# Performance work log

Hardware: AMD Instinct MI355X
Metric: run time of the kernel (lower is better)

## Reference

```python
import jax, jax.numpy as jnp
import numpy as np

N_NODES = 200000
N_EDGES = 600000
FP = 128


def _gru_cell(x, h, wih, whh, bih, bhh):
    # torch.nn.GRUCell: gates ordered (r, z, n)
    gi = x @ wih.T + bih
    gh = h @ whh.T + bhh
    ir, iz, inn = jnp.split(gi, 3, axis=-1)
    hr, hz, hn = jnp.split(gh, 3, axis=-1)
    r = jax.nn.sigmoid(ir + hr)
    z = jax.nn.sigmoid(iz + hz)
    n = jnp.tanh(inn + r * hn)
    return (1.0 - z) * n + z * h


def _layer(x, dst, step, aw, ab, tw, tb, wih, whh, bih, bhh):
    n_nodes = x.shape[0]
    x_i = x[dst]  # [E, F] gather of target-node features
    if step == 0:
        h_s = jnp.broadcast_to(jnp.sum(x_i, axis=-1, keepdims=True), x_i.shape)
    else:
        h_s = x_i
    esv = jax.nn.leaky_relu(jnp.concatenate([h_s, x_i], axis=-1) @ aw.T + ab)  # [E,1]
    asv = jax.nn.softmax(esv, axis=-1)  # size-1 softmax -> ones (faithful)
    cs = jax.nn.elu(asv * (h_s @ tw.T + tb))  # dropout is identity at eval
    m = _gru_cell(cs, h_s, wih, whh, bih, bhh)  # per-edge GRU update [E,F]
    return jax.ops.segment_sum(m, dst, num_segments=n_nodes)  # scatter-add aggregate


def setup_inputs() -> dict:
    key = jax.random.key(0)
    ks = jax.random.split(key, 20)
    s = 1.0 / np.sqrt(FP)
    inp = {
        "x": jax.random.normal(ks[0], (N_NODES, FP), dtype=jnp.float32),
        "edge_index": jax.random.randint(ks[1], (2, N_EDGES), 0, N_NODES, dtype=jnp.int64),
    }
    i = 2
    for l in range(2):
        inp[f"align_w{l}"] = jax.random.uniform(ks[i], (1, 2 * FP), jnp.float32, -s, s); i += 1
        inp[f"align_b{l}"] = jax.random.uniform(ks[i], (1,), jnp.float32, -s, s); i += 1
        inp[f"attend_w{l}"] = jax.random.uniform(ks[i], (FP, FP), jnp.float32, -s, s); i += 1
        inp[f"attend_b{l}"] = jax.random.uniform(ks[i], (FP,), jnp.float32, -s, s); i += 1
        inp[f"wih{l}"] = jax.random.uniform(ks[i], (3 * FP, FP), jnp.float32, -s, s); i += 1
        inp[f"whh{l}"] = jax.random.uniform(ks[i], (3 * FP, FP), jnp.float32, -s, s); i += 1
        inp[f"bih{l}"] = jax.random.uniform(ks[i], (3 * FP,), jnp.float32, -s, s); i += 1
        inp[f"bhh{l}"] = jax.random.uniform(ks[i], (3 * FP,), jnp.float32, -s, s); i += 1
    return inp


def reference(x, edge_index,
              align_w0, align_b0, attend_w0, attend_b0, wih0, whh0, bih0, bhh0,
              align_w1, align_b1, attend_w1, attend_b1, wih1, whh1, bih1, bhh1):
    dst = edge_index[1]
    x = _layer(x, dst, 0, align_w0, align_b0, attend_w0, attend_b0, wih0, whh0, bih0, bhh0)
    x = _layer(x, dst, 1, align_w1, align_b1, attend_w1, attend_b1, wih1, whh1, bih1, bhh1)
    return x
```

## Files before the change

### kernel.cpp

```cpp
#include <hip/hip_runtime.h>
#include <cmath>

#define NN 200000
#define NE 600000

typedef __bf16 bf16x8 __attribute__((ext_vector_type(8)));
typedef float f32x4 __attribute__((ext_vector_type(4)));

#define LOG2E 1.44269504088896340736f
__device__ __forceinline__ float fexp2(float x) { return __builtin_amdgcn_exp2f(x); }
__device__ __forceinline__ float frcp(float x) { return __builtin_amdgcn_rcpf(x); }
__device__ __forceinline__ float sigm(float v) { return frcp(1.0f + fexp2(-LOG2E * v)); }
__device__ __forceinline__ float ftanh(float v) {
  float t = fexp2(-2.0f * LOG2E * fabsf(v));
  float r = (1.0f - t) * frcp(1.0f + t);
  return __builtin_copysignf(r, v);
}
__device__ __forceinline__ float eluf(float v) { return v > 0.0f ? v : fexp2(LOG2E * v) - 1.0f; }

__device__ __forceinline__ unsigned short bfr(float f) {
  unsigned u = __float_as_uint(f);
  u += 0x7FFFu + ((u >> 16) & 1u);
  return (unsigned short)(u >> 16);
}
__device__ __forceinline__ void bsplit(float v, unsigned short& hi, unsigned short& lo) {
  unsigned short h = bfr(v);
  float hf = __uint_as_float(((unsigned)h) << 16);
  hi = h;
  lo = bfr(v - hf);
}


__global__ __launch_bounds__(256) void hist_kernel(const int* __restrict__ dst,
                                                   int* __restrict__ deg) {
  int e = blockIdx.x * 256 + threadIdx.x;
  if (e < NE) atomicAdd(&deg[dst[e]], 1);
}

__global__ __launch_bounds__(512) void prep_kernel(const float* __restrict__ attw0,
                                                   const float* __restrict__ whh0,
                                                   float* __restrict__ rwt0,
                                                   float* __restrict__ rwh0) {
  int t = threadIdx.x;
  if (t < 128) {
    float s = 0.f;
    for (int k = 0; k < 128; k++) s += attw0[t * 128 + k];
    rwt0[t] = s;
  } else {
    int j = t - 128;
    float s = 0.f;
    for (int k = 0; k < 128; k++) s += whh0[j * 128 + k];
    rwh0[j] = s;
  }
}

__global__ __launch_bounds__(256) void pack_kernel(
    const float* __restrict__ wih0, const float* __restrict__ tw1,
    const float* __restrict__ wih1, const float* __restrict__ whh1,
    unsigned short* __restrict__ w0ph, unsigned short* __restrict__ w0pl,
    unsigned short* __restrict__ w1ph, unsigned short* __restrict__ w1pl,
    unsigned short* __restrict__ w2ph, unsigned short* __restrict__ w2pl) {
  int g = blockIdx.x * 256 + threadIdx.x;
  unsigned short *PH, *PL;
  const float* row;
  int l;
  if (g < 6144) { l = g; PH = w0ph; PL = w0pl; }
  else if (g < 8192) { l = g - 6144; PH = w1ph; PL = w1pl; }
  else if (g < 20480) { l = g - 8192; PH = w2ph; PL = w2pl; }
  else return;
  int lane = l & 63, ks = (l >> 6) & 3, nt = l >> 8;
  int n = nt * 16 + (lane & 15);
  int k0 = ks * 32 + (lane >> 4) * 8;
  if (g < 6144) row = wih0 + n * 128;
  else if (g < 8192) row = tw1 + n * 128;
  else row = (n < 384) ? wih1 + n * 128 : whh1 + (n - 384) * 128;
  unsigned uh[4], ul[4];
  for (int p = 0; p < 4; p++) {
    unsigned short ah, al, bh, bl;
    bsplit(row[k0 + 2 * p], ah, al);
    bsplit(row[k0 + 2 * p + 1], bh, bl);
    uh[p] = (unsigned)ah | ((unsigned)bh << 16);
    ul[p] = (unsigned)al | ((unsigned)bl << 16);
  }
  *(uint4*)&PH[l * 8] = make_uint4(uh[0], uh[1], uh[2], uh[3]);
  *(uint4*)&PL[l * 8] = make_uint4(ul[0], ul[1], ul[2], ul[3]);
}

#define MFMA3(accv, ah, al, bh, bl)                                          \
  accv = __builtin_amdgcn_mfma_f32_16x16x32_bf16(ah, bh, accv, 0, 0, 0);     \
  accv = __builtin_amdgcn_mfma_f32_16x16x32_bf16(ah, bl, accv, 0, 0, 0);     \
  accv = __builtin_amdgcn_mfma_f32_16x16x32_bf16(al, bh, accv, 0, 0, 0);

__global__ __launch_bounds__(512, 4) void layer0_kernel(
    const float* __restrict__ x, const float* __restrict__ tb0,
    const unsigned short* __restrict__ w0ph, const unsigned short* __restrict__ w0pl,
    const float* __restrict__ bih0, const float* __restrict__ bhh0,
    const float* __restrict__ rwt0, const float* __restrict__ rwh0,
    const int* __restrict__ deg, float* __restrict__ x1) {
  __shared__ float s_lds[64];
  __shared__ float deg_lds[64];
  __shared__ unsigned short csh[64 * 136];
  __shared__ unsigned short csl[64 * 136];

  const int tid = threadIdx.x;
  const int lane = tid & 63;
  const int wv = tid >> 6;
  const int n0 = blockIdx.x * 64;

  if (tid < 64) deg_lds[tid] = (float)deg[n0 + tid];

  {
    int m = tid >> 3, c = (tid & 7) * 16;
    const float4* xr = (const float4*)(x + (size_t)(n0 + m) * 128 + c);
    float a = 0.f;
#pragma unroll
    for (int q = 0; q < 4; q++) { float4 v = xr[q]; a += v.x + v.y + v.z + v.w; }
#pragma unroll
    for (int o = 1; o < 8; o <<= 1) a += __shfl_xor(a, o, 64);
    if ((tid & 7) == 0) s_lds[m] = a;
  }
  __syncthreads();

  {
    int m = tid >> 3, c0 = (tid & 7) * 16;
    float s = s_lds[m];
#pragma unroll
    for (int q = 0; q < 4; q++) {
      int k = c0 + q * 4;
      unsigned short h0, l0, h1, l1, h2, l2, h3, l3;
      bsplit(eluf(fmaf(s, rwt0[k], tb0[k])), h0, l0);
      bsplit(eluf(fmaf(s, rwt0[k + 1], tb0[k + 1])), h1, l1);
      bsplit(eluf(fmaf(s, rwt0[k + 2], tb0[k + 2])), h2, l2);
      bsplit(eluf(fmaf(s, rwt0[k + 3], tb0[k + 3])), h3, l3);
      *(uint2*)&csh[m * 136 + k] =
          make_uint2((unsigned)h0 | ((unsigned)h1 << 16), (unsigned)h2 | ((unsigned)h3 << 16));
      *(uint2*)&csl[m * 136 + k] =
          make_uint2((unsigned)l0 | ((unsigned)l1 << 16), (unsigned)l2 | ((unsigned)l3 << 16));
    }
  }
  __syncthreads();

  const int mrow = lane & 15;
  const int kq = (lane >> 4) * 8;
  const int quad = lane >> 4;
  f32x4 acc[4][3] = {};
#pragma unroll
  for (int ks = 0; ks < 4; ks++) {
    bf16x8 ah[4], al[4];
#pragma unroll
    for (int mt = 0; mt < 4; mt++) {
      ah[mt] = *(const bf16x8*)&csh[(mt * 16 + mrow) * 136 + ks * 32 + kq];
      al[mt] = *(const bf16x8*)&csl[(mt * 16 + mrow) * 136 + ks * 32 + kq];
    }
#pragma unroll
    for (int g = 0; g < 3; g++) {
      int nt = g * 8 + wv;
      size_t base = (size_t)((nt * 4 + ks) * 64 + lane) * 8;
      bf16x8 bh = *(const bf16x8*)&w0ph[base];
      bf16x8 bl = *(const bf16x8*)&w0pl[base];
#pragma unroll
      for (int mt = 0; mt < 4; mt++) { MFMA3(acc[mt][g], ah[mt], al[mt], bh, bl); }
    }
  }

  const int j = wv * 16 + mrow;
  float bir = bih0[j], biz = bih0[j + 128], bin_ = bih0[j + 256];
  float bhr = bhh0[j], bhz = bhh0[j + 128], bhn = bhh0[j + 256];
  float rwr = rwh0[j], rwz = rwh0[j + 128], rwn = rwh0[j + 256];
#pragma unroll
  for (int mt = 0; mt < 4; mt++) {
#pragma unroll
    for (int reg = 0; reg < 4; reg++) {
      int m = mt * 16 + quad * 4 + reg;
      float s = s_lds[m];
      float dd = deg_lds[m];
      float gir = acc[mt][0][reg] + bir;
      float giz = acc[mt][1][reg] + biz;
      float gin = acc[mt][2][reg] + bin_;
      float ghr = fmaf(s, rwr, bhr);
      float ghz = fmaf(s, rwz, bhz);
      float ghn = fmaf(s, rwn, bhn);
      float r = sigm(gir + ghr);
      float z = sigm(giz + ghz);
      float nn2 = ftanh(fmaf(r, ghn, gin));
      x1[(size_t)(n0 + m) * 128 + j] = dd * ((1.f - z) * nn2 + z * s);
    }
  }
}

__global__ __launch_bounds__(512, 2) void layer1_kernel(
    const float* __restrict__ x1, const float* __restrict__ tb1,
    const unsigned short* __restrict__ w1ph, const unsigned short* __restrict__ w1pl,
    const unsigned short* __restrict__ w2ph, const unsigned short* __restrict__ w2pl,
    const float* __restrict__ bih1, const float* __restrict__ bhh1,
    const int* __restrict__ deg, float* __restrict__ out) {
  extern __shared__ unsigned short smem[];
  unsigned short* hh = smem;
  unsigned short* hl = smem + 8704;
  unsigned short* ch = smem + 17408;
  unsigned short* cl = smem + 26112;
  __shared__ float deg_lds[64];

  const int tid = threadIdx.x;
  const int lane = tid & 63;
  const int wv = tid >> 6;
  const int n0 = blockIdx.x * 64;
  const int mrow = lane & 15;
  const int kq = (lane >> 4) * 8;
  const int quad = lane >> 4;

  if (tid < 64) deg_lds[tid] = (float)deg[n0 + tid];

  {
    int m = tid >> 3, c0 = (tid & 7) * 16;
    const float4* xr = (const float4*)(x1 + (size_t)(n0 + m) * 128 + c0);
#pragma unroll
    for (int q = 0; q < 4; q++) {
      float4 v = xr[q];
      unsigned short h0, l0, h1, l1, h2, l2, h3, l3;
      bsplit(v.x, h0, l0); bsplit(v.y, h1, l1);
      bsplit(v.z, h2, l2); bsplit(v.w, h3, l3);
      *(uint2*)&hh[m * 136 + c0 + q * 4] =
          make_uint2((unsigned)h0 | ((unsigned)h1 << 16), (unsigned)h2 | ((unsigned)h3 << 16));
      *(uint2*)&hl[m * 136 + c0 + q * 4] =
          make_uint2((unsigned)l0 | ((unsigned)l1 << 16), (unsigned)l2 | ((unsigned)l3 << 16));
    }
  }
  __syncthreads();

  f32x4 acc1[4] = {};
  f32x4 acc2[4][6] = {};
#pragma unroll
  for (int ks = 0; ks < 4; ks++) {
    bf16x8 xh[4], xl[4];
#pragma unroll
    for (int mt = 0; mt < 4; mt++) {
      xh[mt] = *(const bf16x8*)&hh[(mt * 16 + mrow) * 136 + ks * 32 + kq];
      xl[mt] = *(const bf16x8*)&hl[(mt * 16 + mrow) * 136 + ks * 32 + kq];
    }
    {
      size_t base = (size_t)((wv * 4 + ks) * 64 + lane) * 8;
      bf16x8 bh = *(const bf16x8*)&w1ph[base];
      bf16x8 bl = *(const bf16x8*)&w1pl[base];
#pragma unroll
      for (int mt = 0; mt < 4; mt++) { MFMA3(acc1[mt], xh[mt], xl[mt], bh, bl); }
    }
#pragma unroll
    for (int g = 0; g < 3; g++) {
      int nt = 24 + g * 8 + wv;
      size_t base = (size_t)((nt * 4 + ks) * 64 + lane) * 8;
      bf16x8 bh = *(const bf16x8*)&w2ph[base];
      bf16x8 bl = *(const bf16x8*)&w2pl[base];
#pragma unroll
      for (int mt = 0; mt < 4; mt++) { MFMA3(acc2[mt][3 + g], xh[mt], xl[mt], bh, bl); }
    }
  }

  {
    float tbj = tb1[wv * 16 + mrow];
#pragma unroll
    for (int mt = 0; mt < 4; mt++) {
#pragma unroll
      for (int reg = 0; reg < 4; reg++) {
        int m = mt * 16 + quad * 4 + reg;
        unsigned short vh, vl;
        bsplit(eluf(acc1[mt][reg] + tbj), vh, vl);
        unsigned pv = (unsigned)vh | ((unsigned)vl << 16);
        unsigned pu = __shfl_xor(pv, 1, 64);
        if ((lane & 1) == 0) {
          int jc = wv * 16 + mrow;
          unsigned hpack = (pv & 0xFFFFu) | (pu << 16);
          unsigned lpack = (pv >> 16) | (pu & 0xFFFF0000u);
          *(unsigned*)&ch[m * 136 + jc] = hpack;
          *(unsigned*)&cl[m * 136 + jc] = lpack;
        }
      }
    }
  }
  __syncthreads();

#pragma unroll
  for (int ks = 0; ks < 4; ks++) {
    bf16x8 ah[4], al[4];
#pragma unroll
    for (int mt = 0; mt < 4; mt++) {
      ah[mt] = *(const bf16x8*)&ch[(mt * 16 + mrow) * 136 + ks * 32 + kq];
      al[mt] = *(const bf16x8*)&cl[(mt * 16 + mrow) * 136 + ks * 32 + kq];
    }
#pragma unroll
    for (int g = 0; g < 3; g++) {
      int nt = g * 8 + wv;
      size_t base = (size_t)((nt * 4 + ks) * 64 + lane) * 8;
      bf16x8 bh = *(const bf16x8*)&w2ph[base];
      bf16x8 bl = *(const bf16x8*)&w2pl[base];
#pragma unroll
      for (int mt = 0; mt < 4; mt++) { MFMA3(acc2[mt][g], ah[mt], al[mt], bh, bl); }
    }
  }

  const int j = wv * 16 + mrow;
  float bir = bih1[j], biz = bih1[j + 128], bin_ = bih1[j + 256];
  float bhr = bhh1[j], bhz = bhh1[j + 128], bhn = bhh1[j + 256];
#pragma unroll
  for (int mt = 0; mt < 4; mt++) {
#pragma unroll
    for (int reg = 0; reg < 4; reg++) {
      int m = mt * 16 + quad * 4 + reg;
      float dd = deg_lds[m];
      float gir = acc2[mt][0][reg] + bir;
      float giz = acc2[mt][1][reg] + biz;
      float gin = acc2[mt][2][reg] + bin_;
      float ghr = acc2[mt][3][reg] + bhr;
      float ghz = acc2[mt][4][reg] + bhz;
      float ghn = acc2[mt][5][reg] + bhn;
      float r = sigm(gir + ghr);
      float z = sigm(giz + ghz);
      float nn2 = ftanh(fmaf(r, ghn, gin));
      float hfull = (float)(*(const __bf16*)&hh[m * 136 + j]) +
                    (float)(*(const __bf16*)&hl[m * 136 + j]);
      out[(size_t)(n0 + m) * 128 + j] = dd * ((1.f - z) * nn2 + z * hfull);
    }
  }
}

extern "C" void kernel_launch(void* const* d_in, const int* in_sizes, int n_in,
                              void* d_out, int out_size, void* d_ws, size_t ws_size,
                              hipStream_t stream) {
  const float* x     = (const float*)d_in[0];
  const int*   edge  = (const int*)d_in[1];
  const float* attw0 = (const float*)d_in[4];
  const float* attb0 = (const float*)d_in[5];
  const float* wih0  = (const float*)d_in[6];
  const float* whh0  = (const float*)d_in[7];
  const float* bih0  = (const float*)d_in[8];
  const float* bhh0  = (const float*)d_in[9];
  const float* attw1 = (const float*)d_in[12];
  const float* attb1 = (const float*)d_in[13];
  const float* wih1  = (const float*)d_in[14];
  const float* whh1  = (const float*)d_in[15];
  const float* bih1  = (const float*)d_in[16];
  const float* bhh1  = (const float*)d_in[17];

  float* ws   = (float*)d_ws;
  float* x1   = ws;
  int*   deg  = (int*)(ws + 25600000);
  float* rwt0 = ws + 25800000;
  float* rwh0 = ws + 25800128;
  unsigned short* wp = (unsigned short*)(ws + 25800512);
  unsigned short* w0ph = wp;
  unsigned short* w0pl = wp + 49152;
  unsigned short* w1ph = wp + 98304;
  unsigned short* w1pl = wp + 114688;
  unsigned short* w2ph = wp + 131072;
  unsigned short* w2pl = wp + 229376;

  const int* dst = edge + NE;

  static bool attr_done = false;
  if (!attr_done) {
    hipFuncSetAttribute(reinterpret_cast<const void*>(layer1_kernel),
                        hipFuncAttributeMaxDynamicSharedMemorySize, 69632);
    attr_done = true;
  }

  hipMemsetAsync(deg, 0, NN * sizeof(int), stream);
  hist_kernel<<<(NE + 255) / 256, 256, 0, stream>>>(dst, deg);
  prep_kernel<<<1, 512, 0, stream>>>(attw0, whh0, rwt0, rwh0);
  pack_kernel<<<80, 256, 0, stream>>>(wih0, attw1, wih1, whh1,
                                      w0ph, w0pl, w1ph, w1pl, w2ph, w2pl);
  layer0_kernel<<<NN / 64, 512, 0, stream>>>(x, attb0, w0ph, w0pl, bih0, bhh0,
                                             rwt0, rwh0, deg, x1);
  layer1_kernel<<<NN / 64, 512, 69632, stream>>>(x1, attb1, w1ph, w1pl, w2ph, w2pl,
                                                 bih1, bhh1, deg, (float*)d_out);
}
```

Measured before the change: 450.1 us.

## Retile layer1 to 128-node blocks with 2D wave grid; parallelize row-sum prep

layer1 now processes 128 nodes per 1024-thread block, with the 16 waves arranged as a 4x4 grid over rows and output columns instead of each wave covering all rows of one column slice. The two GEMMs are interleaved per k-step, and the r/z gates sum the input and hidden accumulators directly, using 4 accumulator groups instead of 6. This is meant to cut weight re-fetches per node and lower register pressure, at the cost of doubling LDS to 136 KB per block, which limits occupancy to one block per CU, and adding tail bounds checks. The one-block prep kernel is also replaced by a wave-per-row shuffle reduction spread over 128 blocks.

```diff
diff --git a/kernel.cpp b/kernel.cpp
--- a/kernel.cpp
+++ b/kernel.cpp
@@ -37,20 +37,21 @@
   if (e < NE) atomicAdd(&deg[dst[e]], 1);
 }
 
-__global__ __launch_bounds__(512) void prep_kernel(const float* __restrict__ attw0,
+__global__ __launch_bounds__(256) void prep_kernel(const float* __restrict__ attw0,
                                                    const float* __restrict__ whh0,
                                                    float* __restrict__ rwt0,
                                                    float* __restrict__ rwh0) {
-  int t = threadIdx.x;
-  if (t < 128) {
-    float s = 0.f;
-    for (int k = 0; k < 128; k++) s += attw0[t * 128 + k];
-    rwt0[t] = s;
-  } else {
-    int j = t - 128;
-    float s = 0.f;
-    for (int k = 0; k < 128; k++) s += whh0[j * 128 + k];
-    rwh0[j] = s;
+  int gw = blockIdx.x * 4 + (threadIdx.x >> 6);
+  int lane = threadIdx.x & 63;
+  const float* row = (gw < 128) ? (attw0 + (size_t)gw * 128)
+                                : (whh0 + (size_t)(gw - 128) * 128);
+  float2 v = ((const float2*)row)[lane];
+  float a = v.x + v.y;
+#pragma unroll
+  for (int o = 1; o < 64; o <<= 1) a += __shfl_xor(a, o, 64);
+  if (lane == 0) {
+    if (gw < 128) rwt0[gw] = a;
+    else rwh0[gw - 128] = a;
   }
 }
 
@@ -188,7 +189,7 @@
   }
 }
 
-__global__ __launch_bounds__(512, 2) void layer1_kernel(
+__global__ __launch_bounds__(1024) void layer1_kernel(
     const float* __restrict__ x1, const float* __restrict__ tb1,
     const unsigned short* __restrict__ w1ph, const unsigned short* __restrict__ w1pl,
     const unsigned short* __restrict__ w2ph, const unsigned short* __restrict__ w2pl,
@@ -196,24 +197,31 @@
     const int* __restrict__ deg, float* __restrict__ out) {
   extern __shared__ unsigned short smem[];
   unsigned short* hh = smem;
-  unsigned short* hl = smem + 8704;
-  unsigned short* ch = smem + 17408;
-  unsigned short* cl = smem + 26112;
-  __shared__ float deg_lds[64];
+  unsigned short* hl = smem + 17408;
+  unsigned short* ch = smem + 34816;
+  unsigned short* cl = smem + 52224;
+  __shared__ float deg_lds[128];
 
   const int tid = threadIdx.x;
   const int lane = tid & 63;
   const int wv = tid >> 6;
-  const int n0 = blockIdx.x * 64;
+  const int mg = wv >> 2;
+  const int ng = wv & 3;
+  const int n0 = blockIdx.x * 128;
   const int mrow = lane & 15;
   const int kq = (lane >> 4) * 8;
   const int quad = lane >> 4;
 
-  if (tid < 64) deg_lds[tid] = (float)deg[n0 + tid];
+  if (tid < 128) {
+    int node = n0 + tid;
+    deg_lds[tid] = (node < NN) ? (float)deg[node] : 0.f;
+  }
 
   {
     int m = tid >> 3, c0 = (tid & 7) * 16;
-    const float4* xr = (const float4*)(x1 + (size_t)(n0 + m) * 128 + c0);
+    int node = n0 + m;
+    if (node >= NN) node = NN - 1;
+    const float4* xr = (const float4*)(x1 + (size_t)node * 128 + c0);
 #pragma unroll
     for (int q = 0; q < 4; q++) {
       float4 v = xr[q];
@@ -228,97 +236,132 @@
   }
   __syncthreads();
 
-  f32x4 acc1[4] = {};
-  f32x4 acc2[4][6] = {};
+  const int r0 = mg * 32;
+  const int c0w = ng * 32;
+
+  f32x4 acc1[2][2] = {};
 #pragma unroll
   for (int ks = 0; ks < 4; ks++) {
-    bf16x8 xh[4], xl[4];
-#pragma unroll
-    for (int mt = 0; mt < 4; mt++) {
-      xh[mt] = *(const bf16x8*)&hh[(mt * 16 + mrow) * 136 + ks * 32 + kq];
-      xl[mt] = *(const bf16x8*)&hl[(mt * 16 + mrow) * 136 + ks * 32 + kq];
-    }
-    {
-      size_t base = (size_t)((wv * 4 + ks) * 64 + lane) * 8;
+    bf16x8 xh[2], xl[2];
+#pragma unroll
+    for (int mt = 0; mt < 2; mt++) {
+      xh[mt] = *(const bf16x8*)&hh[(r0 + mt * 16 + mrow) * 136 + ks * 32 + kq];
+      xl[mt] = *(const bf16x8*)&hl[(r0 + mt * 16 + mrow) * 136 + ks * 32 + kq];
+    }
+#pragma unroll
+    for (int sub = 0; sub < 2; sub++) {
+      int nt = ng * 2 + sub;
+      size_t base = (size_t)((nt * 4 + ks) * 64 + lane) * 8;
       bf16x8 bh = *(const bf16x8*)&w1ph[base];
       bf16x8 bl = *(const bf16x8*)&w1pl[base];
 #pragma unroll
-      for (int mt = 0; mt < 4; mt++) { MFMA3(acc1[mt], xh[mt], xl[mt], bh, bl); }
-    }
-#pragma unroll
-    for (int g = 0; g < 3; g++) {
-      int nt = 24 + g * 8 + wv;
-      size_t base = (size_t)((nt * 4 + ks) * 64 + lane) * 8;
-      bf16x8 bh = *(const bf16x8*)&w2ph[base];
-      bf16x8 bl = *(const bf16x8*)&w2pl[base];
-#pragma unroll
-      for (int mt = 0; mt < 4; mt++) { MFMA3(acc2[mt][3 + g], xh[mt], xl[mt], bh, bl); }
+      for (int mt = 0; mt < 2; mt++) { MFMA3(acc1[mt][sub], xh[mt], xl[mt], bh, bl); }
     }
   }
 
   {
-    float tbj = tb1[wv * 16 + mrow];
-#pragma unroll
-    for (int mt = 0; mt < 4; mt++) {
-#pragma unroll
-      for (int reg = 0; reg < 4; reg++) {
-        int m = mt * 16 + quad * 4 + reg;
-        unsigned short vh, vl;
-        bsplit(eluf(acc1[mt][reg] + tbj), vh, vl);
-        unsigned pv = (unsigned)vh | ((unsigned)vl << 16);
-        unsigned pu = __shfl_xor(pv, 1, 64);
-        if ((lane & 1) == 0) {
-          int jc = wv * 16 + mrow;
-          unsigned hpack = (pv & 0xFFFFu) | (pu << 16);
-          unsigned lpack = (pv >> 16) | (pu & 0xFFFF0000u);
-          *(unsigned*)&ch[m * 136 + jc] = hpack;
-          *(unsigned*)&cl[m * 136 + jc] = lpack;
+    float tbj[2];
+#pragma unroll
+    for (int sub = 0; sub < 2; sub++) tbj[sub] = tb1[c0w + sub * 16 + mrow];
+#pragma unroll
+    for (int mt = 0; mt < 2; mt++) {
+#pragma unroll
+      for (int sub = 0; sub < 2; sub++) {
+#pragma unroll
+        for (int reg = 0; reg < 4; reg++) {
+          int m = r0 + mt * 16 + quad * 4 + reg;
+          unsigned short vh, vl;
+          bsplit(eluf(acc1[mt][sub][reg] + tbj[sub]), vh, vl);
+          unsigned pv = (unsigned)vh | ((unsigned)vl << 16);
+          unsigned pu = __shfl_xor(pv, 1, 64);
+          if ((lane & 1) == 0) {
+            int jc = c0w + sub * 16 + mrow;
+            unsigned hpack = (pv & 0xFFFFu) | (pu << 16);
+            unsigned lpack = (pv >> 16) | (pu & 0xFFFF0000u);
+            *(unsigned*)&ch[m * 136 + jc] = hpack;
+            *(unsigned*)&cl[m * 136 + jc] = lpack;
+          }
         }
       }
     }
   }
   __syncthreads();
 
+  f32x4 acc2[2][2][4] = {};
 #pragma unroll
   for (int ks = 0; ks < 4; ks++) {
-    bf16x8 ah[4], al[4];
-#pragma unroll
-    for (int mt = 0; mt < 4; mt++) {
-      ah[mt] = *(const bf16x8*)&ch[(mt * 16 + mrow) * 136 + ks * 32 + kq];
-      al[mt] = *(const bf16x8*)&cl[(mt * 16 + mrow) * 136 + ks * 32 + kq];
-    }
-#pragma unroll
-    for (int g = 0; g < 3; g++) {
-      int nt = g * 8 + wv;
-      size_t base = (size_t)((nt * 4 + ks) * 64 + lane) * 8;
-      bf16x8 bh = *(const bf16x8*)&w2ph[base];
-      bf16x8 bl = *(const bf16x8*)&w2pl[base];
-#pragma unroll
-      for (int mt = 0; mt < 4; mt++) { MFMA3(acc2[mt][g], ah[mt], al[mt], bh, bl); }
-    }
-  }
-
-  const int j = wv * 16 + mrow;
-  float bir = bih1[j], biz = bih1[j + 128], bin_ = bih1[j + 256];
-  float bhr = bhh1[j], bhz = bhh1[j + 128], bhn = bhh1[j + 256];
-#pragma unroll
-  for (int mt = 0; mt < 4; mt++) {
+    {
+      bf16x8 xh[2], xl[2];
+#pragma unroll
+      for (int mt = 0; mt < 2; mt++) {
+        xh[mt] = *(const bf16x8*)&hh[(r0 + mt * 16 + mrow) * 136 + ks * 32 + kq];
+        xl[mt] = *(const bf16x8*)&hl[(r0 + mt * 16 + mrow) * 136 + ks * 32 + kq];
+      }
+#pragma unroll
+      for (int sub = 0; sub < 2; sub++) {
+#pragma unroll
+        for (int g = 0; g < 3; g++) {
+          int nt = 24 + g * 8 + ng * 2 + sub;
+          size_t base = (size_t)((nt * 4 + ks) * 64 + lane) * 8;
+          bf16x8 bh = *(const bf16x8*)&w2ph[base];
+          bf16x8 bl = *(const bf16x8*)&w2pl[base];
+          int grp = (g == 2) ? 3 : g;
+#pragma unroll
+          for (int mt = 0; mt < 2; mt++) { MFMA3(acc2[mt][sub][grp], xh[mt], xl[mt], bh, bl); }
+        }
+      }
+    }
+    {
+      bf16x8 ah[2], al[2];
+#pragma unroll
+      for (int mt = 0; mt < 2; mt++) {
+        ah[mt] = *(const bf16x8*)&ch[(r0 + mt * 16 + mrow) * 136 + ks * 32 + kq];
+        al[mt] = *(const bf16x8*)&cl[(r0 + mt * 16 + mrow) * 136 + ks * 32 + kq];
+      }
+#pragma unroll
+      for (int sub = 0; sub < 2; sub++) {
+#pragma unroll
+        for (int g = 0; g < 3; g++) {
+          int nt = g * 8 + ng * 2 + sub;
+          size_t base = (size_t)((nt * 4 + ks) * 64 + lane) * 8;
+          bf16x8 bh = *(const bf16x8*)&w2ph[base];
+          bf16x8 bl = *(const bf16x8*)&w2pl[base];
+#pragma unroll
+          for (int mt = 0; mt < 2; mt++) { MFMA3(acc2[mt][sub][g], ah[mt], al[mt], bh, bl); }
+        }
+      }
+    }
+  }
+
+  float bir[2], biz[2], bin_[2], bhr[2], bhz[2], bhn[2];
+  int jcol[2];
+#pragma unroll
+  for (int sub = 0; sub < 2; sub++) {
+    int j = c0w + sub * 16 + mrow;
+    jcol[sub] = j;
+    bir[sub] = bih1[j]; biz[sub] = bih1[j + 128]; bin_[sub] = bih1[j + 256];
+    bhr[sub] = bhh1[j]; bhz[sub] = bhh1[j + 128]; bhn[sub] = bhh1[j + 256];
+  }
+#pragma unroll
+  for (int mt = 0; mt < 2; mt++) {
 #pragma unroll
     for (int reg = 0; reg < 4; reg++) {
-      int m = mt * 16 + quad * 4 + reg;
+      int m = r0 + mt * 16 + quad * 4 + reg;
+      int node = n0 + m;
       float dd = deg_lds[m];
-      float gir = acc2[mt][0][reg] + bir;
-      float giz = acc2[mt][1][reg] + biz;
-      float gin = acc2[mt][2][reg] + bin_;
-      float ghr = acc2[mt][3][reg] + bhr;
-      float ghz = acc2[mt][4][reg] + bhz;
-      float ghn = acc2[mt][5][reg] + bhn;
-      float r = sigm(gir + ghr);
-      float z = sigm(giz + ghz);
-      float nn2 = ftanh(fmaf(r, ghn, gin));
-      float hfull = (float)(*(const __bf16*)&hh[m * 136 + j]) +
-                    (float)(*(const __bf16*)&hl[m * 136 + j]);
-      out[(size_t)(n0 + m) * 128 + j] = dd * ((1.f - z) * nn2 + z * hfull);
+#pragma unroll
+      for (int sub = 0; sub < 2; sub++) {
+        int j = jcol[sub];
+        float r = sigm(acc2[mt][sub][0][reg] + bir[sub] + bhr[sub]);
+        float z = sigm(acc2[mt][sub][1][reg] + biz[sub] + bhz[sub]);
+        float ghn = acc2[mt][sub][3][reg] + bhn[sub];
+        float gin = acc2[mt][sub][2][reg] + bin_[sub];
+        float nn2 = ftanh(fmaf(r, ghn, gin));
+        float hfull = (float)(*(const __bf16*)&hh[m * 136 + j]) +
+                      (float)(*(const __bf16*)&hl[m * 136 + j]);
+        if (node < NN)
+          out[(size_t)node * 128 + j] = dd * ((1.f - z) * nn2 + z * hfull);
+      }
     }
   }
 }
@@ -359,17 +402,17 @@
   static bool attr_done = false;
   if (!attr_done) {
     hipFuncSetAttribute(reinterpret_cast<const void*>(layer1_kernel),
-                        hipFuncAttributeMaxDynamicSharedMemorySize, 69632);
+                        hipFuncAttributeMaxDynamicSharedMemorySize, 139264);
     attr_done = true;
   }
 
   hipMemsetAsync(deg, 0, NN * sizeof(int), stream);
   hist_kernel<<<(NE + 255) / 256, 256, 0, stream>>>(dst, deg);
-  prep_kernel<<<1, 512, 0, stream>>>(attw0, whh0, rwt0, rwh0);
+  prep_kernel<<<128, 256, 0, stream>>>(attw0, whh0, rwt0, rwh0);
   pack_kernel<<<80, 256, 0, stream>>>(wih0, attw1, wih1, whh1,
                                       w0ph, w0pl, w1ph, w1pl, w2ph, w2pl);
   layer0_kernel<<<NN / 64, 512, 0, stream>>>(x, attb0, w0ph, w0pl, bih0, bhh0,
                                              rwt0, rwh0, deg, x1);
-  layer1_kernel<<<NN / 64, 512, 69632, stream>>>(x1, attb1, w1ph, w1pl, w2ph, w2pl,
-                                                 bih1, bhh1, deg, (float*)d_out);
-}
+  layer1_kernel<<<(NN + 127) / 128, 1024, 139264, stream>>>(
+      x1, attb1, w1ph, w1pl, w2ph, w2pl, bih1, bhh1, deg, (float*)d_out);
+}
```

Measured after the change: 489.3 us. 8.7% more time.

## Switch to 32x32x16 MFMA with fragment-packed bf16 hi/lo intermediate layout

Applied to the files above, without the earlier changes.

Replaces the 16x16x32 MFMA tiling with 32x32x16 MFMAs, with each wave computing a 32-row by 32-column tile per gate. Layer 0 now writes its output as split bf16 hi/lo halves, pre-laid out in MFMA A-fragment order. Layer 1 can then load its operands straight from global memory without the LDS staging and bsplit conversion, which cuts LDS use and allows higher occupancy. The prep kernel is also parallelised across many blocks using wave reductions. The cost is extra index arithmetic and a fixed fragment layout in the workspace.

```diff
diff --git a/kernel.cpp b/kernel.cpp
--- a/kernel.cpp
+++ b/kernel.cpp
@@ -5,7 +5,7 @@
 #define NE 600000
 
 typedef __bf16 bf16x8 __attribute__((ext_vector_type(8)));
-typedef float f32x4 __attribute__((ext_vector_type(4)));
+typedef float f32x16 __attribute__((ext_vector_type(16)));
 
 #define LOG2E 1.44269504088896340736f
 __device__ __forceinline__ float fexp2(float x) { return __builtin_amdgcn_exp2f(x); }
@@ -37,20 +37,21 @@
   if (e < NE) atomicAdd(&deg[dst[e]], 1);
 }
 
-__global__ __launch_bounds__(512) void prep_kernel(const float* __restrict__ attw0,
+__global__ __launch_bounds__(256) void prep_kernel(const float* __restrict__ attw0,
                                                    const float* __restrict__ whh0,
                                                    float* __restrict__ rwt0,
                                                    float* __restrict__ rwh0) {
-  int t = threadIdx.x;
-  if (t < 128) {
-    float s = 0.f;
-    for (int k = 0; k < 128; k++) s += attw0[t * 128 + k];
-    rwt0[t] = s;
-  } else {
-    int j = t - 128;
-    float s = 0.f;
-    for (int k = 0; k < 128; k++) s += whh0[j * 128 + k];
-    rwh0[j] = s;
+  int gw = blockIdx.x * 4 + (threadIdx.x >> 6);
+  int lane = threadIdx.x & 63;
+  const float* row = (gw < 128) ? (attw0 + (size_t)gw * 128)
+                                : (whh0 + (size_t)(gw - 128) * 128);
+  float2 v = ((const float2*)row)[lane];
+  float a = v.x + v.y;
+#pragma unroll
+  for (int o = 1; o < 64; o <<= 1) a += __shfl_xor(a, o, 64);
+  if (lane == 0) {
+    if (gw < 128) rwt0[gw] = a;
+    else rwh0[gw - 128] = a;
   }
 }
 
@@ -61,20 +62,21 @@
     unsigned short* __restrict__ w1ph, unsigned short* __restrict__ w1pl,
     unsigned short* __restrict__ w2ph, unsigned short* __restrict__ w2pl) {
   int g = blockIdx.x * 256 + threadIdx.x;
+  if (g >= 20480) return;
   unsigned short *PH, *PL;
   const float* row;
   int l;
   if (g < 6144) { l = g; PH = w0ph; PL = w0pl; }
   else if (g < 8192) { l = g - 6144; PH = w1ph; PL = w1pl; }
-  else if (g < 20480) { l = g - 8192; PH = w2ph; PL = w2pl; }
-  else return;
-  int lane = l & 63, ks = (l >> 6) & 3, nt = l >> 8;
-  int n = nt * 16 + (lane & 15);
-  int k0 = ks * 32 + (lane >> 4) * 8;
+  else { l = g - 8192; PH = w2ph; PL = w2pl; }
+  int lane = l & 63, ks = (l >> 6) & 7, nt = l >> 9;
+  int n = nt * 32 + (lane & 31);
+  int k0 = ks * 16 + (lane >> 5) * 8;
   if (g < 6144) row = wih0 + n * 128;
   else if (g < 8192) row = tw1 + n * 128;
   else row = (n < 384) ? wih1 + n * 128 : whh1 + (n - 384) * 128;
   unsigned uh[4], ul[4];
+#pragma unroll
   for (int p = 0; p < 4; p++) {
     unsigned short ah, al, bh, bl;
     bsplit(row[k0 + 2 * p], ah, al);
@@ -87,24 +89,27 @@
 }
 
 #define MFMA3(accv, ah, al, bh, bl)                                          \
-  accv = __builtin_amdgcn_mfma_f32_16x16x32_bf16(ah, bh, accv, 0, 0, 0);     \
-  accv = __builtin_amdgcn_mfma_f32_16x16x32_bf16(ah, bl, accv, 0, 0, 0);     \
-  accv = __builtin_amdgcn_mfma_f32_16x16x32_bf16(al, bh, accv, 0, 0, 0);
+  accv = __builtin_amdgcn_mfma_f32_32x32x16_bf16(ah, bh, accv, 0, 0, 0);     \
+  accv = __builtin_amdgcn_mfma_f32_32x32x16_bf16(ah, bl, accv, 0, 0, 0);     \
+  accv = __builtin_amdgcn_mfma_f32_32x32x16_bf16(al, bh, accv, 0, 0, 0);
 
 __global__ __launch_bounds__(512, 4) void layer0_kernel(
     const float* __restrict__ x, const float* __restrict__ tb0,
     const unsigned short* __restrict__ w0ph, const unsigned short* __restrict__ w0pl,
     const float* __restrict__ bih0, const float* __restrict__ bhh0,
     const float* __restrict__ rwt0, const float* __restrict__ rwh0,
-    const int* __restrict__ deg, float* __restrict__ x1) {
+    const int* __restrict__ deg,
+    unsigned short* __restrict__ x1h, unsigned short* __restrict__ x1l) {
   __shared__ float s_lds[64];
   __shared__ float deg_lds[64];
-  __shared__ unsigned short csh[64 * 136];
-  __shared__ unsigned short csl[64 * 136];
+  __shared__ unsigned short csh[8192];
+  __shared__ unsigned short csl[8192];
 
   const int tid = threadIdx.x;
   const int lane = tid & 63;
   const int wv = tid >> 6;
+  const int mg = wv & 1;
+  const int cb = wv >> 1;
   const int n0 = blockIdx.x * 64;
 
   if (tid < 64) deg_lds[tid] = (float)deg[n0 + tid];
@@ -122,204 +127,167 @@
   __syncthreads();
 
   {
-    int m = tid >> 3, c0 = (tid & 7) * 16;
+    int m = lane, c = wv;
     float s = s_lds[m];
-#pragma unroll
-    for (int q = 0; q < 4; q++) {
-      int k = c0 + q * 4;
-      unsigned short h0, l0, h1, l1, h2, l2, h3, l3;
-      bsplit(eluf(fmaf(s, rwt0[k], tb0[k])), h0, l0);
-      bsplit(eluf(fmaf(s, rwt0[k + 1], tb0[k + 1])), h1, l1);
-      bsplit(eluf(fmaf(s, rwt0[k + 2], tb0[k + 2])), h2, l2);
-      bsplit(eluf(fmaf(s, rwt0[k + 3], tb0[k + 3])), h3, l3);
-      *(uint2*)&csh[m * 136 + k] =
-          make_uint2((unsigned)h0 | ((unsigned)h1 << 16), (unsigned)h2 | ((unsigned)h3 << 16));
-      *(uint2*)&csl[m * 136 + k] =
-          make_uint2((unsigned)l0 | ((unsigned)l1 << 16), (unsigned)l2 | ((unsigned)l3 << 16));
+    int kb = c * 16;
+    int fb = (((m >> 5) * 8 + c) * 64 + (m & 31)) * 8;
+#pragma unroll
+    for (int u = 0; u < 2; u++) {
+      unsigned uh[4], ul[4];
+#pragma unroll
+      for (int p = 0; p < 4; p++) {
+        int k = kb + u * 8 + p * 2;
+        unsigned short h0, l0, h1, l1;
+        bsplit(eluf(fmaf(s, rwt0[k], tb0[k])), h0, l0);
+        bsplit(eluf(fmaf(s, rwt0[k + 1], tb0[k + 1])), h1, l1);
+        uh[p] = (unsigned)h0 | ((unsigned)h1 << 16);
+        ul[p] = (unsigned)l0 | ((unsigned)l1 << 16);
+      }
+      *(uint4*)&csh[fb + u * 256] = make_uint4(uh[0], uh[1], uh[2], uh[3]);
+      *(uint4*)&csl[fb + u * 256] = make_uint4(ul[0], ul[1], ul[2], ul[3]);
     }
   }
   __syncthreads();
 
-  const int mrow = lane & 15;
-  const int kq = (lane >> 4) * 8;
-  const int quad = lane >> 4;
-  f32x4 acc[4][3] = {};
-#pragma unroll
-  for (int ks = 0; ks < 4; ks++) {
-    bf16x8 ah[4], al[4];
-#pragma unroll
-    for (int mt = 0; mt < 4; mt++) {
-      ah[mt] = *(const bf16x8*)&csh[(mt * 16 + mrow) * 136 + ks * 32 + kq];
-      al[mt] = *(const bf16x8*)&csl[(mt * 16 + mrow) * 136 + ks * 32 + kq];
-    }
+  f32x16 acc[3] = {};
+#pragma unroll
+  for (int ks = 0; ks < 8; ks++) {
+    bf16x8 ah = *(const bf16x8*)&csh[((mg * 8 + ks) * 64 + lane) * 8];
+    bf16x8 al = *(const bf16x8*)&csl[((mg * 8 + ks) * 64 + lane) * 8];
 #pragma unroll
     for (int g = 0; g < 3; g++) {
-      int nt = g * 8 + wv;
-      size_t base = (size_t)((nt * 4 + ks) * 64 + lane) * 8;
+      int nt = g * 4 + cb;
+      size_t base = (size_t)((nt * 8 + ks) * 64 + lane) * 8;
       bf16x8 bh = *(const bf16x8*)&w0ph[base];
       bf16x8 bl = *(const bf16x8*)&w0pl[base];
-#pragma unroll
-      for (int mt = 0; mt < 4; mt++) { MFMA3(acc[mt][g], ah[mt], al[mt], bh, bl); }
-    }
-  }
-
-  const int j = wv * 16 + mrow;
-  float bir = bih0[j], biz = bih0[j + 128], bin_ = bih0[j + 256];
-  float bhr = bhh0[j], bhz = bhh0[j + 128], bhn = bhh0[j + 256];
-  float rwr = rwh0[j], rwz = rwh0[j + 128], rwn = rwh0[j + 256];
-#pragma unroll
-  for (int mt = 0; mt < 4; mt++) {
-#pragma unroll
-    for (int reg = 0; reg < 4; reg++) {
-      int m = mt * 16 + quad * 4 + reg;
-      float s = s_lds[m];
-      float dd = deg_lds[m];
-      float gir = acc[mt][0][reg] + bir;
-      float giz = acc[mt][1][reg] + biz;
-      float gin = acc[mt][2][reg] + bin_;
-      float ghr = fmaf(s, rwr, bhr);
-      float ghz = fmaf(s, rwz, bhz);
-      float ghn = fmaf(s, rwn, bhn);
-      float r = sigm(gir + ghr);
-      float z = sigm(giz + ghz);
-      float nn2 = ftanh(fmaf(r, ghn, gin));
-      x1[(size_t)(n0 + m) * 128 + j] = dd * ((1.f - z) * nn2 + z * s);
-    }
-  }
-}
-
-__global__ __launch_bounds__(512, 2) void layer1_kernel(
-    const float* __restrict__ x1, const float* __restrict__ tb1,
+      MFMA3(acc[g], ah, al, bh, bl);
+    }
+  }
+
+  const int jc = cb * 32 + (lane & 31);
+  float bir = bih0[jc], biz = bih0[jc + 128], bin_ = bih0[jc + 256];
+  float bhr = bhh0[jc], bhz = bhh0[jc + 128], bhn = bhh0[jc + 256];
+  float rwr = rwh0[jc], rwz = rwh0[jc + 128], rwn = rwh0[jc + 256];
+  const size_t tbase = (size_t)blockIdx.x * 8192;
+  const int fj = ((mg * 8 + (cb * 2 + ((lane >> 4) & 1))) * 64 + ((lane >> 3) & 1) * 32) * 8 +
+                 (lane & 7);
+#pragma unroll
+  for (int reg = 0; reg < 16; reg++) {
+    int crow = (reg & 3) + 8 * (reg >> 2) + 4 * (lane >> 5);
+    int m = mg * 32 + crow;
+    float s = s_lds[m];
+    float dd = deg_lds[m];
+    float r = sigm(acc[0][reg] + bir + fmaf(s, rwr, bhr));
+    float z = sigm(acc[1][reg] + biz + fmaf(s, rwz, bhz));
+    float nn2 = ftanh(fmaf(r, fmaf(s, rwn, bhn), acc[2][reg] + bin_));
+    float v = dd * ((1.f - z) * nn2 + z * s);
+    unsigned short vh, vl;
+    bsplit(v, vh, vl);
+    unsigned pv = (unsigned)vh | ((unsigned)vl << 16);
+    unsigned pu = __shfl_xor(pv, 1, 64);
+    if ((lane & 1) == 0) {
+      size_t f = tbase + fj + crow * 8;
+      *(unsigned*)&x1h[f] = (pv & 0xFFFFu) | (pu << 16);
+      *(unsigned*)&x1l[f] = (pv >> 16) | (pu & 0xFFFF0000u);
+    }
+  }
+}
+
+__global__ __launch_bounds__(512, 4) void layer1_kernel(
+    const unsigned short* __restrict__ x1h, const unsigned short* __restrict__ x1l,
+    const float* __restrict__ tb1,
     const unsigned short* __restrict__ w1ph, const unsigned short* __restrict__ w1pl,
     const unsigned short* __restrict__ w2ph, const unsigned short* __restrict__ w2pl,
     const float* __restrict__ bih1, const float* __restrict__ bhh1,
     const int* __restrict__ deg, float* __restrict__ out) {
-  extern __shared__ unsigned short smem[];
-  unsigned short* hh = smem;
-  unsigned short* hl = smem + 8704;
-  unsigned short* ch = smem + 17408;
-  unsigned short* cl = smem + 26112;
+  __shared__ unsigned short cfh[8192];
+  __shared__ unsigned short cfl[8192];
   __shared__ float deg_lds[64];
 
   const int tid = threadIdx.x;
   const int lane = tid & 63;
   const int wv = tid >> 6;
+  const int mg = wv & 1;
+  const int cb = wv >> 1;
   const int n0 = blockIdx.x * 64;
-  const int mrow = lane & 15;
-  const int kq = (lane >> 4) * 8;
-  const int quad = lane >> 4;
+  const size_t tbase = (size_t)blockIdx.x * 8192;
 
   if (tid < 64) deg_lds[tid] = (float)deg[n0 + tid];
 
-  {
-    int m = tid >> 3, c0 = (tid & 7) * 16;
-    const float4* xr = (const float4*)(x1 + (size_t)(n0 + m) * 128 + c0);
-#pragma unroll
-    for (int q = 0; q < 4; q++) {
-      float4 v = xr[q];
-      unsigned short h0, l0, h1, l1, h2, l2, h3, l3;
-      bsplit(v.x, h0, l0); bsplit(v.y, h1, l1);
-      bsplit(v.z, h2, l2); bsplit(v.w, h3, l3);
-      *(uint2*)&hh[m * 136 + c0 + q * 4] =
-          make_uint2((unsigned)h0 | ((unsigned)h1 << 16), (unsigned)h2 | ((unsigned)h3 << 16));
-      *(uint2*)&hl[m * 136 + c0 + q * 4] =
-          make_uint2((unsigned)l0 | ((unsigned)l1 << 16), (unsigned)l2 | ((unsigned)l3 << 16));
-    }
-  }
-  __syncthreads();
-
-  f32x4 acc1[4] = {};
-  f32x4 acc2[4][6] = {};
-#pragma unroll
-  for (int ks = 0; ks < 4; ks++) {
-    bf16x8 xh[4], xl[4];
-#pragma unroll
-    for (int mt = 0; mt < 4; mt++) {
-      xh[mt] = *(const bf16x8*)&hh[(mt * 16 + mrow) * 136 + ks * 32 + kq];
-      xl[mt] = *(const bf16x8*)&hl[(mt * 16 + mrow) * 136 + ks * 32 + kq];
-    }
+  f32x16 aA[4] = {};
+#pragma unroll
+  for (int ks = 0; ks < 8; ks++) {
+    bf16x8 ah = *(const bf16x8*)&x1h[tbase + ((mg * 8 + ks) * 64 + lane) * 8];
+    bf16x8 al = *(const bf16x8*)&x1l[tbase + ((mg * 8 + ks) * 64 + lane) * 8];
     {
-      size_t base = (size_t)((wv * 4 + ks) * 64 + lane) * 8;
+      size_t base = (size_t)((cb * 8 + ks) * 64 + lane) * 8;
       bf16x8 bh = *(const bf16x8*)&w1ph[base];
       bf16x8 bl = *(const bf16x8*)&w1pl[base];
-#pragma unroll
-      for (int mt = 0; mt < 4; mt++) { MFMA3(acc1[mt], xh[mt], xl[mt], bh, bl); }
+      MFMA3(aA[3], ah, al, bh, bl);
     }
 #pragma unroll
     for (int g = 0; g < 3; g++) {
-      int nt = 24 + g * 8 + wv;
-      size_t base = (size_t)((nt * 4 + ks) * 64 + lane) * 8;
+      int nt = 12 + g * 4 + cb;
+      size_t base = (size_t)((nt * 8 + ks) * 64 + lane) * 8;
       bf16x8 bh = *(const bf16x8*)&w2ph[base];
       bf16x8 bl = *(const bf16x8*)&w2pl[base];
-#pragma unroll
-      for (int mt = 0; mt < 4; mt++) { MFMA3(acc2[mt][3 + g], xh[mt], xl[mt], bh, bl); }
+      MFMA3(aA[g], ah, al, bh, bl);
     }
   }
 
   {
-    float tbj = tb1[wv * 16 + mrow];
-#pragma unroll
-    for (int mt = 0; mt < 4; mt++) {
-#pragma unroll
-      for (int reg = 0; reg < 4; reg++) {
-        int m = mt * 16 + quad * 4 + reg;
-        unsigned short vh, vl;
-        bsplit(eluf(acc1[mt][reg] + tbj), vh, vl);
-        unsigned pv = (unsigned)vh | ((unsigned)vl << 16);
-        unsigned pu = __shfl_xor(pv, 1, 64);
-        if ((lane & 1) == 0) {
-          int jc = wv * 16 + mrow;
-          unsigned hpack = (pv & 0xFFFFu) | (pu << 16);
-          unsigned lpack = (pv >> 16) | (pu & 0xFFFF0000u);
-          *(unsigned*)&ch[m * 136 + jc] = hpack;
-          *(unsigned*)&cl[m * 136 + jc] = lpack;
-        }
+    float tbj = tb1[cb * 32 + (lane & 31)];
+    const int fj = ((mg * 8 + (cb * 2 + ((lane >> 4) & 1))) * 64 + ((lane >> 3) & 1) * 32) * 8 +
+                   (lane & 7);
+#pragma unroll
+    for (int reg = 0; reg < 16; reg++) {
+      int crow = (reg & 3) + 8 * (reg >> 2) + 4 * (lane >> 5);
+      unsigned short vh, vl;
+      bsplit(eluf(aA[3][reg] + tbj), vh, vl);
+      unsigned pv = (unsigned)vh | ((unsigned)vl << 16);
+      unsigned pu = __shfl_xor(pv, 1, 64);
+      if ((lane & 1) == 0) {
+        int f = fj + crow * 8;
+        *(unsigned*)&cfh[f] = (pv & 0xFFFFu) | (pu << 16);
+        *(unsigned*)&cfl[f] = (pv >> 16) | (pu & 0xFFFF0000u);
       }
     }
   }
   __syncthreads();
 
-#pragma unroll
-  for (int ks = 0; ks < 4; ks++) {
-    bf16x8 ah[4], al[4];
-#pragma unroll
-    for (int mt = 0; mt < 4; mt++) {
-      ah[mt] = *(const bf16x8*)&ch[(mt * 16 + mrow) * 136 + ks * 32 + kq];
-      al[mt] = *(const bf16x8*)&cl[(mt * 16 + mrow) * 136 + ks * 32 + kq];
-    }
+  f32x16 aB[1] = {};
+#pragma unroll
+  for (int ks = 0; ks < 8; ks++) {
+    bf16x8 ch = *(const bf16x8*)&cfh[((mg * 8 + ks) * 64 + lane) * 8];
+    bf16x8 cl = *(const bf16x8*)&cfl[((mg * 8 + ks) * 64 + lane) * 8];
 #pragma unroll
     for (int g = 0; g < 3; g++) {
-      int nt = g * 8 + wv;
-      size_t base = (size_t)((nt * 4 + ks) * 64 + lane) * 8;
+      int nt = g * 4 + cb;
+      size_t base = (size_t)((nt * 8 + ks) * 64 + lane) * 8;
       bf16x8 bh = *(const bf16x8*)&w2ph[base];
       bf16x8 bl = *(const bf16x8*)&w2pl[base];
-#pragma unroll
-      for (int mt = 0; mt < 4; mt++) { MFMA3(acc2[mt][g], ah[mt], al[mt], bh, bl); }
-    }
-  }
-
-  const int j = wv * 16 + mrow;
-  float bir = bih1[j], biz = bih1[j + 128], bin_ = bih1[j + 256];
-  float bhr = bhh1[j], bhz = bhh1[j + 128], bhn = bhh1[j + 256];
-#pragma unroll
-  for (int mt = 0; mt < 4; mt++) {
-#pragma unroll
-    for (int reg = 0; reg < 4; reg++) {
-      int m = mt * 16 + quad * 4 + reg;
-      float dd = deg_lds[m];
-      float gir = acc2[mt][0][reg] + bir;
-      float giz = acc2[mt][1][reg] + biz;
-      float gin = acc2[mt][2][reg] + bin_;
-      float ghr = acc2[mt][3][reg] + bhr;
-      float ghz = acc2[mt][4][reg] + bhz;
-      float ghn = acc2[mt][5][reg] + bhn;
-      float r = sigm(gir + ghr);
-      float z = sigm(giz + ghz);
-      float nn2 = ftanh(fmaf(r, ghn, gin));
-      float hfull = (float)(*(const __bf16*)&hh[m * 136 + j]) +
-                    (float)(*(const __bf16*)&hl[m * 136 + j]);
-      out[(size_t)(n0 + m) * 128 + j] = dd * ((1.f - z) * nn2 + z * hfull);
-    }
+      if (g == 0) { MFMA3(aA[0], ch, cl, bh, bl); }
+      else if (g == 1) { MFMA3(aA[1], ch, cl, bh, bl); }
+      else { MFMA3(aB[0], ch, cl, bh, bl); }
+    }
+  }
+
+  const int jc = cb * 32 + (lane & 31);
+  float bir = bih1[jc], biz = bih1[jc + 128], bin_ = bih1[jc + 256];
+  float bhr = bhh1[jc], bhz = bhh1[jc + 128], bhn = bhh1[jc + 256];
+  const int fj = ((mg * 8 + (cb * 2 + ((lane >> 4) & 1))) * 64 + ((lane >> 3) & 1) * 32) * 8 +
+                 (lane & 7);
+#pragma unroll
+  for (int reg = 0; reg < 16; reg++) {
+    int crow = (reg & 3) + 8 * (reg >> 2) + 4 * (lane >> 5);
+    int m = mg * 32 + crow;
+    float dd = deg_lds[m];
+    float r = sigm(aA[0][reg] + bir + bhr);
+    float z = sigm(aA[1][reg] + biz + bhz);
+    float nn2 = ftanh(fmaf(r, aA[2][reg] + bhn, aB[0][reg] + bin_));
+    size_t f = tbase + fj + crow * 8;
+    float hfull = (float)(*(const __bf16*)&x1h[f]) + (float)(*(const __bf16*)&x1l[f]);
+    out[(size_t)(n0 + m) * 128 + jc] = dd * ((1.f - z) * nn2 + z * hfull);
   }
 }
 
@@ -341,8 +309,9 @@
   const float* bih1  = (const float*)d_in[16];
   const float* bhh1  = (const float*)d_in[17];
 
-  float* ws   = (float*)d_ws;
-  float* x1   = ws;
+  float* ws = (float*)d_ws;
+  unsigned short* x1h = (unsigned short*)ws;
+  unsigned short* x1l = (unsigned short*)(ws + 12800000);
   int*   deg  = (int*)(ws + 25600000);
   float* rwt0 = ws + 25800000;
   float* rwh0 = ws + 25800128;
@@ -356,20 +325,13 @@
 
   const int* dst = edge + NE;
 
-  static bool attr_done = false;
-  if (!attr_done) {
-    hipFuncSetAttribute(reinterpret_cast<const void*>(layer1_kernel),
-                        hipFuncAttributeMaxDynamicSharedMemorySize, 69632);
-    attr_done = true;
-  }
-
   hipMemsetAsync(deg, 0, NN * sizeof(int), stream);
   hist_kernel<<<(NE + 255) / 256, 256, 0, stream>>>(dst, deg);
-  prep_kernel<<<1, 512, 0, stream>>>(attw0, whh0, rwt0, rwh0);
+  prep_kernel<<<128, 256, 0, stream>>>(attw0, whh0, rwt0, rwh0);
   pack_kernel<<<80, 256, 0, stream>>>(wih0, attw1, wih1, whh1,
                                       w0ph, w0pl, w1ph, w1pl, w2ph, w2pl);
   layer0_kernel<<<NN / 64, 512, 0, stream>>>(x, attb0, w0ph, w0pl, bih0, bhh0,
-                                             rwt0, rwh0, deg, x1);
-  layer1_kernel<<<NN / 64, 512, 69632, stream>>>(x1, attb1, w1ph, w1pl, w2ph, w2pl,
-                                                 bih1, bhh1, deg, (float*)d_out);
-}
+                                             rwt0, rwh0, deg, x1h, x1l);
+  layer1_kernel<<<NN / 64, 512, 0, stream>>>(x1h, x1l, attb1, w1ph, w1pl, w2ph, w2pl,
+                                             bih1, bhh1, deg, (float*)d_out);
+}
```

Measured after the change: 473.8 us. 1.05x slower.
